# Kernel optimization log

Hardware: AMD Instinct MI355X
Metric: run time of the kernel (lower is better)

The kernel has to match this reference:

```python
import jax, jax.numpy as jnp
import numpy as np

CUTOFF = 6.0   # dist_hard_max
BOX = 20.0     # cubic cell edge (Angstrom)
N_IMAGES = 1   # floor(CUTOFF/BOX + eps) + 1 per axis for this cell


def setup_inputs() -> dict:
    key = jax.random.key(0)
    M, N = 8, 400
    coordinates = jax.random.uniform(key, (M, N, 3), dtype=jnp.float32) * BOX
    cell = jnp.tile((BOX * jnp.eye(3, dtype=jnp.float32))[None], (M, 1, 1))
    return {"coordinates": coordinates, "cell": cell}


def reference(coordinates, cell):
    # coordinates: [M, N, 3]; cell: [M, 3, 3]
    M, N, _ = coordinates.shape
    inv_cell = jnp.linalg.inv(cell)                                   # [M,3,3]
    proj = jnp.einsum('mnd,mde->mne', coordinates, inv_cell)          # fractional coords
    wrap_off = jnp.floor(proj)                                        # [M,N,3] wrapped_offset
    wrapped = coordinates - jnp.einsum('mne,med->mnd', wrap_off, cell)  # wrapped coords

    # all image offsets in [-N_IMAGES, N_IMAGES]^3 (27 images)
    rng = jnp.arange(-N_IMAGES, N_IMAGES + 1)
    images = jnp.stack(jnp.meshgrid(rng, rng, rng, indexing='ij'), axis=-1).reshape(-1, 3)  # [K,3]

    shift = jnp.einsum('kc,mcd->mkd', images.astype(cell.dtype), cell)  # [M,K,3]
    drij = wrapped[:, :, None, :] - wrapped[:, None, :, :]              # [M,N,N,3]
    # paircoord[m,k,i,j] = r_i - r_j + image_k @ cell  (identical to torch paircoord values)
    paircoord = drij[:, None] + shift[:, :, None, None, :]             # [M,K,N,N,3]
    d2 = jnp.sum(paircoord * paircoord, axis=-1)                       # [M,K,N,N]

    eye = jnp.eye(N, dtype=bool)
    zero_img = jnp.all(images == 0, axis=-1)                           # [K]
    mask = (d2 < CUTOFF ** 2) & ~(zero_img[None, :, None, None] & eye[None, None, :, :])
    dist = jnp.where(mask, jnp.sqrt(jnp.where(mask, d2, 1.0)), 0.0)    # safe sqrt

    # pair_image = image - (wrap_off_i - wrap_off_j); offset_index as in torch forward
    wo = wrap_off.astype(jnp.int32)
    wij = wo[:, :, None, :] - wo[:, None, :, :]                        # [M,N,N,3]
    pair_image = images.astype(jnp.int32)[None, :, None, None, :] - wij[:, None]  # [M,K,N,N,3]
    n_off = 2 * N_IMAGES + 1
    o = pair_image + N_IMAGES
    offset_index = o[..., 2] + n_off * (o[..., 1] + n_off * o[..., 0])  # [M,K,N,N]

    paircoord_masked = jnp.where(mask[..., None], paircoord, 0.0)
    return dist, paircoord_masked, mask, offset_index
```

## Files before the change

### kernel.cpp

```cpp
#include <hip/hip_runtime.h>

constexpr int M = 8;
constexpr int N = 400;
constexpr int K = 27;
constexpr float CUT2 = 36.0f;
constexpr int D  = M * K * N * N;
constexpr int F4 = D / 4;

typedef float f32x4 __attribute__((ext_vector_type(4)));

constexpr int WS_WRAPPED = 0;
constexpr int WS_WO      = 38400;
constexpr int WS_SHIFT   = 76800;

__global__ __launch_bounds__(128)
void setup_kernel(const float* __restrict__ coords, const float* __restrict__ cell,
                  float* __restrict__ wrapped, int* __restrict__ wo,
                  float* __restrict__ shift)
{
    int m = blockIdx.x;
    const float* c = cell + m * 9;
    float c00 = c[0], c01 = c[1], c02 = c[2];
    float c10 = c[3], c11 = c[4], c12 = c[5];
    float c20 = c[6], c21 = c[7], c22 = c[8];

    float det = c00 * (c11 * c22 - c12 * c21)
              - c01 * (c10 * c22 - c12 * c20)
              + c02 * (c10 * c21 - c11 * c20);
    float rd = 1.0f / det;
    float i00 = (c11 * c22 - c12 * c21) * rd, i01 = (c02 * c21 - c01 * c22) * rd, i02 = (c01 * c12 - c02 * c11) * rd;
    float i10 = (c12 * c20 - c10 * c22) * rd, i11 = (c00 * c22 - c02 * c20) * rd, i12 = (c02 * c10 - c00 * c12) * rd;
    float i20 = (c10 * c21 - c11 * c20) * rd, i21 = (c01 * c20 - c00 * c21) * rd, i22 = (c00 * c11 - c01 * c10) * rd;

    for (int n = threadIdx.x; n < N; n += blockDim.x) {
        int b = (m * N + n) * 3;
        float x = coords[b + 0], y = coords[b + 1], z = coords[b + 2];
        float p0 = x * i00 + y * i10 + z * i20;
        float p1 = x * i01 + y * i11 + z * i21;
        float p2 = x * i02 + y * i12 + z * i22;
        float f0 = floorf(p0), f1 = floorf(p1), f2 = floorf(p2);
        wrapped[b + 0] = x - (f0 * c00 + f1 * c10 + f2 * c20);
        wrapped[b + 1] = y - (f0 * c01 + f1 * c11 + f2 * c21);
        wrapped[b + 2] = z - (f0 * c02 + f1 * c12 + f2 * c22);
        wo[b + 0] = (int)f0;
        wo[b + 1] = (int)f1;
        wo[b + 2] = (int)f2;
    }

    if (threadIdx.x < K) {
        int k = threadIdx.x;
        float fx = (float)(k / 9 - 1);
        float fy = (float)((k / 3) % 3 - 1);
        float fz = (float)(k % 3 - 1);
        int sb = (m * K + k) * 3;
        shift[sb + 0] = fx * c00 + fy * c10 + fz * c20;
        shift[sb + 1] = fx * c01 + fy * c11 + fz * c21;
        shift[sb + 2] = fx * c02 + fy * c12 + fz * c22;
    }
}

__global__ __launch_bounds__(256)
void pairs_kernel(const float* __restrict__ wrapped, const int* __restrict__ wo,
                  const float* __restrict__ shift, float* __restrict__ out)
{
    __shared__ f32x4 lds[3][257];

    int tid = threadIdx.x;
    int t = blockIdx.x * 256 + tid;
    int jq = t % (N / 4);
    int r  = t / (N / 4);
    int i  = r % N;
    int mk = r / N;
    int k  = mk % K;
    int m  = mk / K;
    int j0 = 4 * jq;

    const float4* w4 = reinterpret_cast<const float4*>(wrapped + m * (N * 3)) + 3 * jq;
    float4 wa = w4[0], wb = w4[1], wc = w4[2];
    float wjx[4] = { wa.x, wa.w, wb.z, wc.y };
    float wjy[4] = { wa.y, wb.x, wb.w, wc.z };
    float wjz[4] = { wa.z, wb.y, wc.x, wc.w };

    const int4* o4j = reinterpret_cast<const int4*>(wo + m * (N * 3)) + 3 * jq;
    int4 oa = o4j[0], ob = o4j[1], oc = o4j[2];
    int ojx[4] = { oa.x, oa.w, ob.z, oc.y };
    int ojy[4] = { oa.y, ob.x, ob.w, oc.z };
    int ojz[4] = { oa.z, ob.y, oc.x, oc.w };

    int ib = m * (N * 3) + 3 * i;
    float wix = wrapped[ib], wiy = wrapped[ib + 1], wiz = wrapped[ib + 2];
    int   oix = wo[ib],      oiy = wo[ib + 1],      oiz = wo[ib + 2];
    float sx = shift[mk * 3], sy = shift[mk * 3 + 1], sz = shift[mk * 3 + 2];
    int imx = k / 9 - 1, imy = (k / 3) % 3 - 1, imz = k % 3 - 1;

    float dist[4], msk[4], offv[4], pc[12];
    #pragma unroll
    for (int dj = 0; dj < 4; ++dj) {
        float px = __fadd_rn(__fsub_rn(wix, wjx[dj]), sx);
        float py = __fadd_rn(__fsub_rn(wiy, wjy[dj]), sy);
        float pz = __fadd_rn(__fsub_rn(wiz, wjz[dj]), sz);
        float d2 = __fadd_rn(__fadd_rn(__fmul_rn(px, px), __fmul_rn(py, py)),
                             __fmul_rn(pz, pz));
        bool mb = (d2 < CUT2) && !((k == (K / 2)) && (i == j0 + dj));
        dist[dj] = mb ? sqrtf(d2) : 0.0f;
        msk[dj]  = mb ? 1.0f : 0.0f;
        pc[3 * dj + 0] = mb ? px : 0.0f;
        pc[3 * dj + 1] = mb ? py : 0.0f;
        pc[3 * dj + 2] = mb ? pz : 0.0f;
        int ox = imx - (oix - ojx[dj]) + 1;
        int oy = imy - (oiy - ojy[dj]) + 1;
        int oz = imz - (oiz - ojz[dj]) + 1;
        offv[dj] = (float)(oz + 3 * (oy + 3 * ox));
    }

    f32x4* out4 = reinterpret_cast<f32x4*>(out);
    f32x4 dv = { dist[0], dist[1], dist[2], dist[3] };
    f32x4 mv = { msk[0],  msk[1],  msk[2],  msk[3]  };
    f32x4 ov = { offv[0], offv[1], offv[2], offv[3] };
    f32x4 p0 = { pc[0], pc[1], pc[2],  pc[3]  };
    f32x4 p1 = { pc[4], pc[5], pc[6],  pc[7]  };
    f32x4 p2 = { pc[8], pc[9], pc[10], pc[11] };

    out4[t] = dv;
    out4[4 * F4 + t] = mv;
    out4[5 * F4 + t] = ov;

    lds[0][tid] = p0;
    lds[1][tid] = p1;
    lds[2][tid] = p2;
    __syncthreads();
    int base = F4 + 3 * (blockIdx.x * 256);
    #pragma unroll
    for (int rr = 0; rr < 3; ++rr) {
        int idx = rr * 256 + tid;
        int s = idx / 3;
        int q = idx - 3 * s;
        out4[base + idx] = lds[q][s];
    }
}

extern "C" void kernel_launch(void* const* d_in, const int* in_sizes, int n_in,
                              void* d_out, int out_size, void* d_ws, size_t ws_size,
                              hipStream_t stream) {
    const float* coords = (const float*)d_in[0];
    const float* cell   = (const float*)d_in[1];
    float* out = (float*)d_out;

    char* ws = (char*)d_ws;
    float* wrapped = (float*)(ws + WS_WRAPPED);
    int*   wo      = (int*)  (ws + WS_WO);
    float* shift   = (float*)(ws + WS_SHIFT);

    setup_kernel<<<M, 128, 0, stream>>>(coords, cell, wrapped, wo, shift);

    int total = M * K * N * (N / 4);
    int blocks = total / 256;
    pairs_kernel<<<blocks, 256, 0, stream>>>(wrapped, wo, shift, out);
}
```

Baseline: 802.0 us.

## Use persistent grid-stride blocks and per-wave LDS transpose without block barrier

The pairs kernel now launches a fixed grid of persistent blocks that loop over tiles instead of one block per tile. The paircoord transpose through shared memory is split per wavefront, so the block-wide barrier becomes wave-local waitcnt instructions. The aim is to cut launch and block-scheduling overhead and barrier stalls in this store-bound kernel. Relying on intra-wave lockstep with raw s_waitcnt is fragile, and the fixed grid size may underfill or unbalance the GPU.

New measurement: 811.5 us. No clear change (+1.2%).

```diff
diff --git a/kernel.cpp b/kernel.cpp
--- a/kernel.cpp
+++ b/kernel.cpp
@@ -6,6 +6,8 @@
 constexpr float CUT2 = 36.0f;
 constexpr int D  = M * K * N * N;
 constexpr int F4 = D / 4;
+constexpr int TILES = M * K * N * (N / 4) / 256;
+constexpr int NBLOCKS = 2048;
 
 typedef float f32x4 __attribute__((ext_vector_type(4)));
 
@@ -63,79 +65,85 @@
 void pairs_kernel(const float* __restrict__ wrapped, const int* __restrict__ wo,
                   const float* __restrict__ shift, float* __restrict__ out)
 {
-    __shared__ f32x4 lds[3][257];
+    __shared__ f32x4 lds[4][3][65];
 
-    int tid = threadIdx.x;
-    int t = blockIdx.x * 256 + tid;
-    int jq = t % (N / 4);
-    int r  = t / (N / 4);
-    int i  = r % N;
-    int mk = r / N;
-    int k  = mk % K;
-    int m  = mk / K;
-    int j0 = 4 * jq;
+    int tid  = threadIdx.x;
+    int wave = tid >> 6;
+    int lane = tid & 63;
+    f32x4* out4 = reinterpret_cast<f32x4*>(out);
 
-    const float4* w4 = reinterpret_cast<const float4*>(wrapped + m * (N * 3)) + 3 * jq;
-    float4 wa = w4[0], wb = w4[1], wc = w4[2];
-    float wjx[4] = { wa.x, wa.w, wb.z, wc.y };
-    float wjy[4] = { wa.y, wb.x, wb.w, wc.z };
-    float wjz[4] = { wa.z, wb.y, wc.x, wc.w };
+    for (int tile = blockIdx.x; tile < TILES; tile += NBLOCKS) {
+        int t = tile * 256 + tid;
+        int jq = t % (N / 4);
+        int r  = t / (N / 4);
+        int i  = r % N;
+        int mk = r / N;
+        int k  = mk % K;
+        int m  = mk / K;
+        int j0 = 4 * jq;
 
-    const int4* o4j = reinterpret_cast<const int4*>(wo + m * (N * 3)) + 3 * jq;
-    int4 oa = o4j[0], ob = o4j[1], oc = o4j[2];
-    int ojx[4] = { oa.x, oa.w, ob.z, oc.y };
-    int ojy[4] = { oa.y, ob.x, ob.w, oc.z };
-    int ojz[4] = { oa.z, ob.y, oc.x, oc.w };
+        const float4* w4 = reinterpret_cast<const float4*>(wrapped + m * (N * 3)) + 3 * jq;
+        float4 wa = w4[0], wb = w4[1], wc = w4[2];
+        float wjx[4] = { wa.x, wa.w, wb.z, wc.y };
+        float wjy[4] = { wa.y, wb.x, wb.w, wc.z };
+        float wjz[4] = { wa.z, wb.y, wc.x, wc.w };
 
-    int ib = m * (N * 3) + 3 * i;
-    float wix = wrapped[ib], wiy = wrapped[ib + 1], wiz = wrapped[ib + 2];
-    int   oix = wo[ib],      oiy = wo[ib + 1],      oiz = wo[ib + 2];
-    float sx = shift[mk * 3], sy = shift[mk * 3 + 1], sz = shift[mk * 3 + 2];
-    int imx = k / 9 - 1, imy = (k / 3) % 3 - 1, imz = k % 3 - 1;
+        const int4* o4j = reinterpret_cast<const int4*>(wo + m * (N * 3)) + 3 * jq;
+        int4 oa = o4j[0], ob = o4j[1], oc = o4j[2];
+        int ojx[4] = { oa.x, oa.w, ob.z, oc.y };
+        int ojy[4] = { oa.y, ob.x, ob.w, oc.z };
+        int ojz[4] = { oa.z, ob.y, oc.x, oc.w };
 
-    float dist[4], msk[4], offv[4], pc[12];
-    #pragma unroll
-    for (int dj = 0; dj < 4; ++dj) {
-        float px = __fadd_rn(__fsub_rn(wix, wjx[dj]), sx);
-        float py = __fadd_rn(__fsub_rn(wiy, wjy[dj]), sy);
-        float pz = __fadd_rn(__fsub_rn(wiz, wjz[dj]), sz);
-        float d2 = __fadd_rn(__fadd_rn(__fmul_rn(px, px), __fmul_rn(py, py)),
-                             __fmul_rn(pz, pz));
-        bool mb = (d2 < CUT2) && !((k == (K / 2)) && (i == j0 + dj));
-        dist[dj] = mb ? sqrtf(d2) : 0.0f;
-        msk[dj]  = mb ? 1.0f : 0.0f;
-        pc[3 * dj + 0] = mb ? px : 0.0f;
-        pc[3 * dj + 1] = mb ? py : 0.0f;
-        pc[3 * dj + 2] = mb ? pz : 0.0f;
-        int ox = imx - (oix - ojx[dj]) + 1;
-        int oy = imy - (oiy - ojy[dj]) + 1;
-        int oz = imz - (oiz - ojz[dj]) + 1;
-        offv[dj] = (float)(oz + 3 * (oy + 3 * ox));
-    }
+        int ib = m * (N * 3) + 3 * i;
+        float wix = wrapped[ib], wiy = wrapped[ib + 1], wiz = wrapped[ib + 2];
+        int   oix = wo[ib],      oiy = wo[ib + 1],      oiz = wo[ib + 2];
+        float sx = shift[mk * 3], sy = shift[mk * 3 + 1], sz = shift[mk * 3 + 2];
+        int imx = k / 9 - 1, imy = (k / 3) % 3 - 1, imz = k % 3 - 1;
 
-    f32x4* out4 = reinterpret_cast<f32x4*>(out);
-    f32x4 dv = { dist[0], dist[1], dist[2], dist[3] };
-    f32x4 mv = { msk[0],  msk[1],  msk[2],  msk[3]  };
-    f32x4 ov = { offv[0], offv[1], offv[2], offv[3] };
-    f32x4 p0 = { pc[0], pc[1], pc[2],  pc[3]  };
-    f32x4 p1 = { pc[4], pc[5], pc[6],  pc[7]  };
-    f32x4 p2 = { pc[8], pc[9], pc[10], pc[11] };
+        float dist[4], msk[4], offv[4], pc[12];
+        #pragma unroll
+        for (int dj = 0; dj < 4; ++dj) {
+            float px = __fadd_rn(__fsub_rn(wix, wjx[dj]), sx);
+            float py = __fadd_rn(__fsub_rn(wiy, wjy[dj]), sy);
+            float pz = __fadd_rn(__fsub_rn(wiz, wjz[dj]), sz);
+            float d2 = __fadd_rn(__fadd_rn(__fmul_rn(px, px), __fmul_rn(py, py)),
+                                 __fmul_rn(pz, pz));
+            bool mb = (d2 < CUT2) && !((k == (K / 2)) && (i == j0 + dj));
+            dist[dj] = mb ? sqrtf(d2) : 0.0f;
+            msk[dj]  = mb ? 1.0f : 0.0f;
+            pc[3 * dj + 0] = mb ? px : 0.0f;
+            pc[3 * dj + 1] = mb ? py : 0.0f;
+            pc[3 * dj + 2] = mb ? pz : 0.0f;
+            int ox = imx - (oix - ojx[dj]) + 1;
+            int oy = imy - (oiy - ojy[dj]) + 1;
+            int oz = imz - (oiz - ojz[dj]) + 1;
+            offv[dj] = (float)(oz + 3 * (oy + 3 * ox));
+        }
 
-    out4[t] = dv;
-    out4[4 * F4 + t] = mv;
-    out4[5 * F4 + t] = ov;
+        f32x4 dv = { dist[0], dist[1], dist[2], dist[3] };
+        f32x4 mv = { msk[0],  msk[1],  msk[2],  msk[3]  };
+        f32x4 ov = { offv[0], offv[1], offv[2], offv[3] };
 
-    lds[0][tid] = p0;
-    lds[1][tid] = p1;
-    lds[2][tid] = p2;
-    __syncthreads();
-    int base = F4 + 3 * (blockIdx.x * 256);
-    #pragma unroll
-    for (int rr = 0; rr < 3; ++rr) {
-        int idx = rr * 256 + tid;
-        int s = idx / 3;
-        int q = idx - 3 * s;
-        out4[base + idx] = lds[q][s];
+        out4[t] = dv;
+        out4[4 * F4 + t] = mv;
+        out4[5 * F4 + t] = ov;
+
+        asm volatile("s_waitcnt lgkmcnt(0)" ::: "memory");
+
+        lds[wave][0][lane] = f32x4{ pc[0], pc[1], pc[2],  pc[3]  };
+        lds[wave][1][lane] = f32x4{ pc[4], pc[5], pc[6],  pc[7]  };
+        lds[wave][2][lane] = f32x4{ pc[8], pc[9], pc[10], pc[11] };
+
+        asm volatile("s_waitcnt lgkmcnt(0)" ::: "memory");
+
+        int base4 = F4 + 3 * (tile * 256 + wave * 64);
+        #pragma unroll
+        for (int rr = 0; rr < 3; ++rr) {
+            int idx = rr * 64 + lane;
+            int s = idx / 3;
+            int q = idx - 3 * s;
+            out4[base4 + idx] = lds[wave][q][s];
+        }
     }
 }
 
@@ -152,8 +160,5 @@
     float* shift   = (float*)(ws + WS_SHIFT);
 
     setup_kernel<<<M, 128, 0, stream>>>(coords, cell, wrapped, wo, shift);
-
-    int total = M * K * N * (N / 4);
-    int blocks = total / 256;
-    pairs_kernel<<<blocks, 256, 0, stream>>>(wrapped, wo, shift, out);
+    pairs_kernel<<<NBLOCKS, 256, 0, stream>>>(wrapped, wo, shift, out);
 }
```
